# Optimization experiments

Measured on AMD Instinct MI355X. Metric: run time of the kernel, lower is better.

The kernel has to match this reference:

```python
import jax, jax.numpy as jnp
import numpy as np

B, S, E, H = 2, 2048, 1024, 16
DK = E // H
THRESHOLD = 0.1


def setup_inputs() -> dict:
    key = jax.random.key(0)
    ks = jax.random.split(key, 11)
    s = 1.0 / np.sqrt(E)
    return {
        "queries": jax.random.normal(ks[0], (B, S, E), jnp.float32),
        "keys": jax.random.normal(ks[1], (B, S, E), jnp.float32),
        "values": jax.random.normal(ks[2], (B, S, E), jnp.float32),
        "Wq": jax.random.normal(ks[3], (E, E), jnp.float32) * s,
        "bq": jnp.zeros((E,), jnp.float32),
        "Wk": jax.random.normal(ks[4], (E, E), jnp.float32) * s,
        "bk": jnp.zeros((E,), jnp.float32),
        "Wv": jax.random.normal(ks[5], (E, E), jnp.float32) * s,
        "bv": jnp.zeros((E,), jnp.float32),
        "Wp": jax.random.normal(ks[6], (E, E), jnp.float32) * s,
        "bp": jnp.zeros((E,), jnp.float32),
    }


def _split(x):
    # [B,S,E] -> [B,H,S,dk]
    return x.reshape(B, S, H, DK).transpose(0, 2, 1, 3)


def reference(queries, keys, values, Wq, bq, Wk, bk, Wv, bv, Wp, bp):
    q = _split(queries @ Wq.T + bq)
    k = _split(keys @ Wk.T + bk)
    v = _split(values @ Wv.T + bv)
    logits = jnp.einsum("bhsd,bhtd->bhst", q, k) / np.sqrt(DK)
    probs = jax.nn.softmax(logits, axis=-1)                    # [B,H,S,S]
    mask = (probs > THRESHOLD).astype(probs.dtype)
    # straight-through: value = mask*probs, grads flow via (mask*probs + probs)
    thr = mask * probs - jax.lax.stop_gradient(probs) + probs
    hidden = jnp.einsum("bhst,bhtd->bhsd", thr, v)             # [B,H,S,dk]
    merged = hidden.transpose(0, 2, 1, 3).reshape(B, S, E)
    out = merged @ Wp.T + bp
    adjacency = probs.mean(axis=1)                             # avg_attn_heads=True
    return (out, adjacency)
```

## Files before the change

### kernel.cpp

```cpp
#include <hip/hip_runtime.h>
#include <cstddef>
#include <cstdint>

constexpr size_t OUT_ELEMS = (size_t)2 * 2048 * 1024;

typedef _Float16 f16_t;
typedef __attribute__((ext_vector_type(8))) _Float16 f16x8;
typedef __attribute__((ext_vector_type(4))) float f32x4;

#define SCL2      0.1803368801111204f
#define LOG2_0P1  -3.3219280948873623f

#define EXP2F(x)  __builtin_amdgcn_exp2f(x)
#define LOG2F(x)  __builtin_amdgcn_logf(x)

#define WAITV(N)  asm volatile("s_waitcnt vmcnt(" #N ")" ::: "memory")
__device__ __forceinline__ void ringbar() {
    __builtin_amdgcn_s_barrier();
    __builtin_amdgcn_sched_barrier(0);
}

__device__ __forceinline__ f32x4 mfma16(f16x8 a, f16x8 b, f32x4 c) {
    return __builtin_amdgcn_mfma_f32_16x16x32_f16(a, b, c, 0, 0, 0);
}

__device__ __forceinline__ void gload16(const void* g, void* l) {
    __builtin_amdgcn_global_load_lds(
        (const __attribute__((address_space(1))) void*)g,
        (__attribute__((address_space(3))) void*)l, 16, 0, 0);
}

__global__ __launch_bounds__(256)
void prep_kernel(const float4* __restrict__ q, const float4* __restrict__ k,
                 const float4* __restrict__ v, const float4* __restrict__ wq,
                 const float4* __restrict__ wk, const float4* __restrict__ wv,
                 const float4* __restrict__ wp,
                 unsigned short* __restrict__ xq, unsigned short* __restrict__ xk,
                 unsigned short* __restrict__ xv, unsigned short* __restrict__ wqh,
                 unsigned short* __restrict__ wkh, unsigned short* __restrict__ wvh,
                 unsigned short* __restrict__ wph)
{
    const int z = blockIdx.y;
    const int i = blockIdx.x * 256 + threadIdx.x;
    const float4* src; unsigned short* dst; int total4;
    switch (z) {
        case 0:  src = q;  dst = xq;  total4 = 1048576; break;
        case 1:  src = k;  dst = xk;  total4 = 1048576; break;
        case 2:  src = v;  dst = xv;  total4 = 1048576; break;
        case 3:  src = wq; dst = wqh; total4 = 262144;  break;
        case 4:  src = wk; dst = wkh; total4 = 262144;  break;
        case 5:  src = wv; dst = wvh; total4 = 262144;  break;
        default: src = wp; dst = wph; total4 = 262144;  break;
    }
    if (i >= total4) return;
    const float4 v4 = src[i];
    const float vv[4] = {v4.x, v4.y, v4.z, v4.w};
    unsigned short u[4];
#pragma unroll
    for (int j = 0; j < 4; ++j) {
        f16_t h = (f16_t)vv[j];
        u[j] = __builtin_bit_cast(unsigned short, h);
    }
    uint2 w;
    w.x = u[0] | ((unsigned)u[1] << 16); w.y = u[2] | ((unsigned)u[3] << 16);
    *(uint2*)(dst + (size_t)i * 4) = w;
}

template<int OUTMODE>
__global__ __launch_bounds__(512)
void gemm_mfma(const f16_t* __restrict__ A, const f16_t* __restrict__ B,
               const float* __restrict__ bias, float scaleB,
               float* __restrict__ outF, f16_t* __restrict__ outB,
               const unsigned* __restrict__ dmask)
{
    __shared__ __align__(16) char Asl[3][16384];
    __shared__ __align__(16) char Bsl[3][16384];

    const int tid = threadIdx.x;
    const int lane = tid & 63;
    const int w = tid >> 6;
    const int wm = w >> 1;
    const int wn = w & 1;
    const int n0 = blockIdx.x * 128;
    const int m0 = blockIdx.y * 128;

    if (OUTMODE == 2) {
        const int bb = m0 >> 11;
        const int st0 = (m0 & 2047) >> 6;
        unsigned dd = 0;
        for (int hh = 0; hh < 16; ++hh)
            dd |= dmask[(bb * 16 + hh) * 32 + st0] | dmask[(bb * 16 + hh) * 32 + st0 + 1];
        if (dd == 0u) {
            const int row = tid >> 2;
            const int c0 = (tid & 3) * 32;
            float* dst = outF + (size_t)(m0 + row) * 1024 + n0 + c0;
#pragma unroll
            for (int j = 0; j < 8; ++j)
                *(float4*)(dst + j * 4) = *(const float4*)(bias + n0 + c0 + j * 4);
            return;
        }
    }

    f32x4 acc[2][4] = {};

    auto stage = [&](int ki, int buf) {
        const int kt = ki * 64;
#pragma unroll
        for (int inst = 0; inst < 2; ++inst) {
            int L = inst * 8192 + tid * 16;
            int row = L >> 7;
            int k16 = ((L >> 4) & 7) ^ (row & 7);
            gload16(A + (size_t)(m0 + row) * 1024 + kt + k16 * 8,
                    Asl[buf] + inst * 8192 + w * 1024);
            gload16(B + (size_t)(n0 + row) * 1024 + kt + k16 * 8,
                    Bsl[buf] + inst * 8192 + w * 1024);
        }
    };

    stage(0, 0);

    for (int ki = 0; ki < 16; ++ki) {
        if (ki + 1 < 16) stage(ki + 1, (ki + 1) % 3);
        if (ki < 15) { WAITV(4); } else { WAITV(0); }
        ringbar();
        const char* Ab = Asl[ki % 3];
        const char* Bb = Bsl[ki % 3];
#pragma unroll
        for (int kf = 0; kf < 2; ++kf) {
            const int k16 = kf * 4 + (lane >> 4);
            f16x8 af[2], bfr[4];
#pragma unroll
            for (int mi = 0; mi < 2; ++mi) {
                int row = wm * 32 + mi * 16 + (lane & 15);
                af[mi] = *(const f16x8*)(Ab + (row << 7) + ((k16 ^ (row & 7)) << 4));
            }
#pragma unroll
            for (int ni = 0; ni < 4; ++ni) {
                int row = wn * 64 + ni * 16 + (lane & 15);
                bfr[ni] = *(const f16x8*)(Bb + (row << 7) + ((k16 ^ (row & 7)) << 4));
            }
#pragma unroll
            for (int mi = 0; mi < 2; ++mi)
#pragma unroll
                for (int ni = 0; ni < 4; ++ni)
                    acc[mi][ni] = mfma16(af[mi], bfr[ni], acc[mi][ni]);
        }
    }

    const int crow0 = wm * 32 + (lane >> 4) * 4;
    const int ccol0 = wn * 64 + (lane & 15);
#pragma unroll
    for (int mi = 0; mi < 2; ++mi) {
#pragma unroll
        for (int ni = 0; ni < 4; ++ni) {
            const int n = n0 + ccol0 + ni * 16;
            const float bb = bias[n];
            if (OUTMODE == 2) {
#pragma unroll
                for (int r = 0; r < 4; ++r) {
                    const int m = m0 + crow0 + mi * 16 + r;
                    outF[(size_t)m * 1024 + n] = acc[mi][ni][r] + bb;
                }
            } else if (OUTMODE == 0) {
                const int h = n >> 6, d = n & 63;
#pragma unroll
                for (int r = 0; r < 4; ++r) {
                    const int m = m0 + crow0 + mi * 16 + r;
                    const int b = m >> 11, s = m & 2047;
                    const float v = acc[mi][ni][r] + bb;
                    const size_t idx = ((size_t)(b * 16 + h) * 2048 + s) * 64 + d;
                    outB[idx] = (f16_t)(v * scaleB);
                    outF[idx] = v;
                }
            } else {
                const int h = n >> 6, d = n & 63;
                const int m = m0 + crow0 + mi * 16;
                const int b = m >> 11, s = m & 2047;
                unsigned short us[4];
#pragma unroll
                for (int r = 0; r < 4; ++r) {
                    f16_t t = (f16_t)(acc[mi][ni][r] + bb);
                    us[r] = __builtin_bit_cast(unsigned short, t);
                }
                uint2 pk;
                pk.x = us[0] | ((unsigned)us[1] << 16);
                pk.y = us[2] | ((unsigned)us[3] << 16);
                *(uint2*)(outB + ((size_t)(b * 16 + h) * 64 + d) * 2048 + s) = pk;
            }
        }
    }
}

__global__ __launch_bounds__(512)
void attn_zsweep_kernel(const f16_t* __restrict__ qh, const f16_t* __restrict__ kh,
                        float2* __restrict__ partials)
{
    __shared__ __align__(16) char Klds[16384];

    const int tid = threadIdx.x;
    const int lane = tid & 63;
    const int g = lane >> 4;
    const int w = tid >> 6;
    const int tc = blockIdx.x;
    const int bh = blockIdx.y;

    {
        const size_t kbase = ((size_t)bh * 2048 + tc * 128) * 64;
#pragma unroll
        for (int inst = 0; inst < 2; ++inst) {
            int L = inst * 8192 + tid * 16;
            int row = L >> 7;
            int k16 = ((L >> 4) & 7) ^ (row & 7);
            gload16(kh + kbase + (size_t)row * 64 + k16 * 8,
                    Klds + inst * 8192 + w * 1024);
        }
    }
    __syncthreads();

    auto qload = [&](int si, f16x8& a, f16x8& b) {
        const size_t rb = ((size_t)bh * 2048 + si * 128 + w * 16 + (lane & 15)) * 64;
        a = *(const f16x8*)(qh + rb + g * 8);
        b = *(const f16x8*)(qh + rb + 32 + g * 8);
    };

    auto compute = [&](int si, f16x8 q0, f16x8 q1) {
        f32x4 acc[8] = {};
#pragma unroll
        for (int kf = 0; kf < 2; ++kf) {
            const f16x8 qf = kf ? q1 : q0;
            const int k16 = kf * 4 + g;
#pragma unroll
            for (int tg = 0; tg < 8; ++tg) {
                const int t = tg * 16 + (lane & 15);
                f16x8 bfr = *(const f16x8*)(Klds + (t << 7) + ((k16 ^ (t & 7)) << 4));
                acc[tg] = mfma16(qf, bfr, acc[tg]);
            }
        }
#pragma unroll
        for (int r = 0; r < 4; ++r) {
            float sm = 0.0f, mx = -1e30f;
#pragma unroll
            for (int tg = 0; tg < 8; ++tg) {
                const float l2 = acc[tg][r];
                sm += EXP2F(l2);
                mx = fmaxf(mx, l2);
            }
#pragma unroll
            for (int mk = 1; mk < 16; mk <<= 1) {
                sm += __shfl_xor(sm, mk);
                mx = fmaxf(mx, __shfl_xor(mx, mk));
            }
            if ((lane & 15) == 0) {
                const int srow = si * 128 + w * 16 + g * 4 + r;
                partials[((size_t)bh * 2048 + srow) * 16 + tc] = make_float2(sm, mx);
            }
        }
    };

    f16x8 qA0, qA1, qB0, qB1;
    qload(0, qA0, qA1);
    for (int si = 0; si < 16; si += 2) {
        qload(si + 1, qB0, qB1);
        compute(si, qA0, qA1);
        if (si + 2 < 16) qload(si + 2, qA0, qA1);
        compute(si + 1, qB0, qB1);
    }
}

__global__ __launch_bounds__(256)
void zred_kernel(const float2* __restrict__ partials, float* __restrict__ stats,
                 unsigned* __restrict__ dirtymask)
{
    const int tid = threadIdx.x;
    const int bh = blockIdx.y;
    const int s = blockIdx.x * 256 + tid;
    const float4* p = (const float4*)(partials + ((size_t)bh * 2048 + s) * 16);
    float sm = 0.0f, mx = -1e30f;
#pragma unroll
    for (int i = 0; i < 8; ++i) {
        const float4 v = p[i];
        sm += v.x + v.z;
        mx = fmaxf(mx, fmaxf(v.y, v.w));
    }
    const float lgZ = LOG2F(sm);
    stats[(size_t)bh * 2048 + s] = lgZ;
    const bool dirty = mx > lgZ + LOG2_0P1 - 0.10f;
    const unsigned long long m = __ballot(dirty);
    if ((tid & 63) == 0)
        dirtymask[bh * 32 + (s >> 6)] = (m != 0ull) ? 1u : 0u;
}

__global__ __launch_bounds__(256)
void attn_pv_kernel(const f16_t* __restrict__ qh, const f16_t* __restrict__ kh,
                    const f16_t* __restrict__ vT,
                    const float* __restrict__ qf32, const float* __restrict__ kf32,
                    const float* __restrict__ stats, const unsigned* __restrict__ dirtymask,
                    const float2* __restrict__ partials,
                    f16_t* __restrict__ merged)
{
    __shared__ __align__(16) char Klds[8192];
    __shared__ __align__(16) char Vlds[8192];
    __shared__ __align__(16) char Pl[4][2048];
    __shared__ unsigned cflags;

    const int tid = threadIdx.x;
    const int lane = tid & 63;
    const int g = lane >> 4;
    const int w = tid >> 6;
    const int s0 = blockIdx.x * 64;
    const int bh = blockIdx.y;
    const int b = bh >> 4, h = bh & 15;

    if (dirtymask[bh * 32 + blockIdx.x] == 0u) {
        const int row = s0 + (tid >> 2);
        f16_t* dst = merged + ((size_t)b * 2048 + row) * 1024 + h * 64 + (tid & 3) * 16;
        const uint4 z = {0u, 0u, 0u, 0u};
        *(uint4*)dst = z;
        *(uint4*)(dst + 8) = z;
        return;
    }

    f16x8 qf[2];
    float lgZ[4], lthr[4];
    {
        const size_t rowbase = ((size_t)bh * 2048 + s0 + w * 16 + (lane & 15)) * 64;
        qf[0] = *(const f16x8*)(qh + rowbase + g * 8);
        qf[1] = *(const f16x8*)(qh + rowbase + 32 + g * 8);
#pragma unroll
        for (int r = 0; r < 4; ++r) {
            lgZ[r] = stats[(size_t)bh * 2048 + s0 + w * 16 + g * 4 + r];
            lthr[r] = lgZ[r] + LOG2_0P1;
        }
    }

    if (tid == 0) cflags = 0u;
    __syncthreads();
    {
        unsigned f = 0;
#pragma unroll
        for (int r = 0; r < 4; ++r) {
            const size_t rowg = (size_t)bh * 2048 + s0 + w * 16 + g * 4 + r;
            const float thr = lthr[r] - 0.10f;
#pragma unroll
            for (int tc = 0; tc < 16; ++tc)
                if (partials[rowg * 16 + tc].y > thr) f |= (1u << tc);
        }
        if (f) atomicOr(&cflags, f);
    }
    __syncthreads();
    const unsigned flags = cflags;

    const size_t kbase = (size_t)bh * 2048 * 64;
    const size_t vbase = (size_t)bh * 64 * 2048;

    f32x4 hacc[4] = {};
    for (int tcc = 0; tcc < 2048; tcc += 64) {
        if (!((flags >> (tcc >> 7)) & 1u)) continue;
#pragma unroll
        for (int inst = 0; inst < 2; ++inst) {
            int L = inst * 4096 + tid * 16;
            int t = L >> 7;
            int k16 = ((L >> 4) & 7) ^ (t & 7);
            gload16(kh + kbase + (size_t)(tcc + t) * 64 + k16 * 8,
                    Klds + inst * 4096 + w * 1024);
            int d = t;
            gload16(vT + vbase + (size_t)d * 2048 + tcc + k16 * 8,
                    Vlds + inst * 4096 + w * 1024);
        }
        __syncthreads();

        f32x4 acc[4] = {};
#pragma unroll
        for (int kf = 0; kf < 2; ++kf) {
            const int k16 = kf * 4 + g;
            f16x8 bfr[4];
#pragma unroll
            for (int tg = 0; tg < 4; ++tg) {
                int t = tg * 16 + (lane & 15);
                bfr[tg] = *(const f16x8*)(Klds + (t << 7) + ((k16 ^ (t & 7)) << 4));
            }
#pragma unroll
            for (int tg = 0; tg < 4; ++tg)
                acc[tg] = mfma16(qf[kf], bfr[tg], acc[tg]);
        }

        char* pb = Pl[w];
        bool any = false;
#pragma unroll
        for (int tg = 0; tg < 4; ++tg)
#pragma unroll
            for (int r = 0; r < 4; ++r) {
                const float l2 = acc[tg][r];
                float p = 0.0f;
                if (l2 > lthr[r] - 0.07f) {
                    if (fabsf(l2 - lthr[r]) < 0.07f) {
                        const float* qr = qf32 + ((size_t)bh * 2048 + s0 + w * 16 + g * 4 + r) * 64;
                        const float* kr = kf32 + ((size_t)bh * 2048 + tcc + tg * 16 + (lane & 15)) * 64;
                        float dt = 0.0f;
                        for (int dd = 0; dd < 64; ++dd) dt += qr[dd] * kr[dd];
                        const float pe = EXP2F(dt * SCL2 - lgZ[r]);
                        p = (pe > 0.1f) ? pe : 0.0f;
                    } else {
                        p = EXP2F(l2 - lgZ[r]);
                    }
                }
                any |= (p != 0.0f);
                const int row = g * 4 + r;
                const int t = tg * 16 + (lane & 15);
                *(f16_t*)(pb + (row << 7) + ((2 * t) ^ ((row & 7) << 4))) = (f16_t)p;
            }

        if (__ballot(any) != 0ull) {
#pragma unroll
            for (int kf = 0; kf < 2; ++kf) {
                const int t16 = kf * 4 + g;
                f16x8 pa, vb[4];
                {
                    const int row = lane & 15;
                    pa = *(const f16x8*)(pb + (row << 7) + ((t16 ^ (row & 7)) << 4));
                }
#pragma unroll
                for (int ni = 0; ni < 4; ++ni) {
                    const int d = ni * 16 + (lane & 15);
                    vb[ni] = *(const f16x8*)(Vlds + (d << 7) + ((t16 ^ (d & 7)) << 4));
                }
#pragma unroll
                for (int ni = 0; ni < 4; ++ni)
                    hacc[ni] = mfma16(pa, vb[ni], hacc[ni]);
            }
        }
        __syncthreads();
    }

#pragma unroll
    for (int ni = 0; ni < 4; ++ni)
#pragma unroll
        for (int r = 0; r < 4; ++r) {
            const int srow = s0 + w * 16 + g * 4 + r;
            const int col = h * 64 + ni * 16 + (lane & 15);
            merged[((size_t)b * 2048 + srow) * 1024 + col] = (f16_t)hacc[ni][r];
        }
}

__global__ __launch_bounds__(256, 4)
void attn_adj_kernel(const f16_t* __restrict__ qh, const f16_t* __restrict__ kh,
                     const float* __restrict__ stats, float* __restrict__ adj)
{
    __shared__ __align__(16) char Klds[2][16384];
    __shared__ __align__(16) float Sl[16 * 64];

    const int tid = threadIdx.x;
    const int lane = tid & 63;
    const int g = lane >> 4;
    const int w = tid >> 6;
    const int t0 = blockIdx.x * 128;
    const int s0 = blockIdx.y * 64;
    const int b  = blockIdx.z;

    {
        const int hh = tid >> 4;
        const int sl = (tid * 4) & 63;
        const float4 v = *(const float4*)(stats + ((size_t)(b * 16 + hh) * 2048 + s0 + sl));
        *(float4*)&Sl[tid * 4] = v;
    }

    auto stageK = [&](int h, int buf) {
        const size_t kbase = ((size_t)(b * 16 + h) * 2048 + t0) * 64;
#pragma unroll
        for (int inst = 0; inst < 4; ++inst) {
            int L = inst * 4096 + tid * 16;
            int row = L >> 7;
            int k16 = ((L >> 4) & 7) ^ (row & 7);
            gload16(kh + kbase + (size_t)row * 64 + k16 * 8,
                    Klds[buf] + inst * 4096 + w * 1024);
        }
    };

    f32x4 aacc[8] = {};

    stageK(0, 0);
    __syncthreads();

    for (int h = 0; h < 16; ++h) {
        if (h + 1 < 16) stageK(h + 1, (h + 1) & 1);

        f16x8 q0, q1;
        {
            const size_t rb = ((size_t)(b * 16 + h) * 2048 + s0 + w * 16 + (lane & 15)) * 64;
            q0 = *(const f16x8*)(qh + rb + g * 8);
            q1 = *(const f16x8*)(qh + rb + 32 + g * 8);
        }
        float cc[4];
#pragma unroll
        for (int r = 0; r < 4; ++r)
            cc[r] = Sl[h * 64 + w * 16 + g * 4 + r] + 4.0f;

        const char* Kb = Klds[h & 1];
        f32x4 acc[8] = {};
#pragma unroll
        for (int kf = 0; kf < 2; ++kf) {
            const f16x8 qf = kf ? q1 : q0;
            const int k16 = kf * 4 + g;
#pragma unroll
            for (int tg = 0; tg < 8; ++tg) {
                const int t = tg * 16 + (lane & 15);
                const f16x8 bfr = *(const f16x8*)(Kb + (t << 7) + ((k16 ^ (t & 7)) << 4));
                acc[tg] = mfma16(qf, bfr, acc[tg]);
            }
        }
#pragma unroll
        for (int tg = 0; tg < 8; ++tg)
#pragma unroll
            for (int r = 0; r < 4; ++r)
                aacc[tg][r] += EXP2F(acc[tg][r] - cc[r]);

        __syncthreads();
    }

#pragma unroll
    for (int tg = 0; tg < 8; ++tg)
#pragma unroll
        for (int r = 0; r < 4; ++r) {
            const int s = s0 + w * 16 + g * 4 + r;
            adj[((size_t)b * 2048 + s) * 2048 + t0 + tg * 16 + (lane & 15)] = aacc[tg][r];
        }
}

extern "C" void kernel_launch(void* const* d_in, const int* in_sizes, int n_in,
                              void* d_out, int out_size, void* d_ws, size_t ws_size,
                              hipStream_t stream)
{
    (void)in_sizes; (void)n_in; (void)out_size; (void)ws_size;

    const float* queries = (const float*)d_in[0];
    const float* keys    = (const float*)d_in[1];
    const float* values  = (const float*)d_in[2];
    const float* Wq = (const float*)d_in[3];
    const float* bq = (const float*)d_in[4];
    const float* Wk = (const float*)d_in[5];
    const float* bk = (const float*)d_in[6];
    const float* Wv = (const float*)d_in[7];
    const float* bv = (const float*)d_in[8];
    const float* Wp = (const float*)d_in[9];
    const float* bp = (const float*)d_in[10];

    float* out = (float*)d_out;
    float* adj = out + OUT_ELEMS;

    char* ws = (char*)d_ws;
    f16_t* Xq   = (f16_t*)(ws);
    f16_t* Xk   = (f16_t*)(ws + 8388608);
    f16_t* Xv   = (f16_t*)(ws + 16777216);
    f16_t* Wqh  = (f16_t*)(ws + 25165824);
    f16_t* Wkh  = (f16_t*)(ws + 27262976);
    f16_t* Wvh  = (f16_t*)(ws + 29360128);
    f16_t* Wph  = (f16_t*)(ws + 31457280);
    f16_t* qh16 = (f16_t*)(ws + 33554432);
    f16_t* kh16 = (f16_t*)(ws + 41943040);
    f16_t* vT   = (f16_t*)(ws + 50331648);
    f16_t* mg   = (f16_t*)(ws + 58720256);
    float* qf32 = (float*)(ws + 67108864);
    float* kf32 = (float*)(ws + 83886080);
    float* stats = (float*)(ws + 100663296);
    float2* partials  = (float2*)(ws);
    unsigned* dirtymask = (unsigned*)(ws + 16777216 + 4194304);

    prep_kernel<<<dim3(4096, 7), 256, 0, stream>>>(
        (const float4*)queries, (const float4*)keys, (const float4*)values,
        (const float4*)Wq, (const float4*)Wk, (const float4*)Wv, (const float4*)Wp,
        (unsigned short*)Xq, (unsigned short*)Xk, (unsigned short*)Xv,
        (unsigned short*)Wqh, (unsigned short*)Wkh, (unsigned short*)Wvh,
        (unsigned short*)Wph);

    const dim3 gg(8, 32);
    gemm_mfma<0><<<gg, 512, 0, stream>>>(Xq, Wqh, bq, SCL2, qf32, qh16, nullptr);
    gemm_mfma<0><<<gg, 512, 0, stream>>>(Xk, Wkh, bk, 1.0f, kf32, kh16, nullptr);
    gemm_mfma<1><<<gg, 512, 0, stream>>>(Xv, Wvh, bv, 1.0f, nullptr, vT, nullptr);

    attn_zsweep_kernel<<<dim3(16, 32), 512, 0, stream>>>(qh16, kh16, partials);
    zred_kernel<<<dim3(8, 32), 256, 0, stream>>>(partials, stats, dirtymask);
    attn_pv_kernel<<<dim3(32, 32), 256, 0, stream>>>(qh16, kh16, vT, qf32, kf32,
                                                     stats, dirtymask, partials, mg);
    attn_adj_kernel<<<dim3(16, 32, 2), 256, 0, stream>>>(qh16, kh16, stats, adj);

    gemm_mfma<2><<<gg, 512, 0, stream>>>(mg, Wph, bp, 1.0f, out, nullptr, dirtymask);
}
```

Before: 168.2 us.

## Hold K tiles in registers for score sweeps and refine skip granularity

The row-sum sweep kernel and the adjacency kernel now keep K fragments in registers instead of staging them through LDS, which removes the shared-memory staging and the barriers. The sweep uses swapped MFMA operands so the reductions need fewer shuffles. The sweep also splits keys into 64-wide slices instead of 128-wide, so partials grow to 32 per row. The PV kernel can then skip 64-key chunks individually. The cost is more partial-statistic traffic and more redundant global Q/K loads per block in the adjacency kernel, which leans on L2.

```diff
diff --git a/kernel.cpp b/kernel.cpp
--- a/kernel.cpp
+++ b/kernel.cpp
@@ -191,70 +191,59 @@
     }
 }
 
-__global__ __launch_bounds__(512)
+__global__ __launch_bounds__(512, 4)
 void attn_zsweep_kernel(const f16_t* __restrict__ qh, const f16_t* __restrict__ kh,
                         float2* __restrict__ partials)
 {
-    __shared__ __align__(16) char Klds[16384];
-
     const int tid = threadIdx.x;
     const int lane = tid & 63;
     const int g = lane >> 4;
     const int w = tid >> 6;
-    const int tc = blockIdx.x;
-    const int bh = blockIdx.y;
-
-    {
-        const size_t kbase = ((size_t)bh * 2048 + tc * 128) * 64;
-#pragma unroll
-        for (int inst = 0; inst < 2; ++inst) {
-            int L = inst * 8192 + tid * 16;
-            int row = L >> 7;
-            int k16 = ((L >> 4) & 7) ^ (row & 7);
-            gload16(kh + kbase + (size_t)row * 64 + k16 * 8,
-                    Klds + inst * 8192 + w * 1024);
-        }
-    }
-    __syncthreads();
+    const int ts = w & 3;
+    const int sh = w >> 2;
+    const int t0 = blockIdx.x * 256 + ts * 64;
+    const int s0 = blockIdx.y * 512 + sh * 256;
+    const int bh = blockIdx.z;
+    const int slice = blockIdx.x * 4 + ts;
+
+    f16x8 kreg[2][4];
+#pragma unroll
+    for (int kf = 0; kf < 2; ++kf)
+#pragma unroll
+        for (int tg = 0; tg < 4; ++tg)
+            kreg[kf][tg] = *(const f16x8*)(kh +
+                ((size_t)bh * 2048 + t0 + tg * 16 + (lane & 15)) * 64 + kf * 32 + g * 8);
 
     auto qload = [&](int si, f16x8& a, f16x8& b) {
-        const size_t rb = ((size_t)bh * 2048 + si * 128 + w * 16 + (lane & 15)) * 64;
+        const size_t rb = ((size_t)bh * 2048 + s0 + si * 16 + (lane & 15)) * 64;
         a = *(const f16x8*)(qh + rb + g * 8);
         b = *(const f16x8*)(qh + rb + 32 + g * 8);
     };
 
     auto compute = [&](int si, f16x8 q0, f16x8 q1) {
-        f32x4 acc[8] = {};
-#pragma unroll
-        for (int kf = 0; kf < 2; ++kf) {
-            const f16x8 qf = kf ? q1 : q0;
-            const int k16 = kf * 4 + g;
-#pragma unroll
-            for (int tg = 0; tg < 8; ++tg) {
-                const int t = tg * 16 + (lane & 15);
-                f16x8 bfr = *(const f16x8*)(Klds + (t << 7) + ((k16 ^ (t & 7)) << 4));
-                acc[tg] = mfma16(qf, bfr, acc[tg]);
-            }
-        }
-#pragma unroll
-        for (int r = 0; r < 4; ++r) {
-            float sm = 0.0f, mx = -1e30f;
-#pragma unroll
-            for (int tg = 0; tg < 8; ++tg) {
-                const float l2 = acc[tg][r];
-                sm += EXP2F(l2);
-                mx = fmaxf(mx, l2);
-            }
-#pragma unroll
-            for (int mk = 1; mk < 16; mk <<= 1) {
-                sm += __shfl_xor(sm, mk);
-                mx = fmaxf(mx, __shfl_xor(mx, mk));
-            }
-            if ((lane & 15) == 0) {
-                const int srow = si * 128 + w * 16 + g * 4 + r;
-                partials[((size_t)bh * 2048 + srow) * 16 + tc] = make_float2(sm, mx);
-            }
-        }
+        f32x4 acc[4] = {};
+#pragma unroll
+        for (int tg = 0; tg < 4; ++tg) {
+            acc[tg] = mfma16(kreg[0][tg], q0, acc[tg]);
+            acc[tg] = mfma16(kreg[1][tg], q1, acc[tg]);
+        }
+        float sms[4] = {0.0f, 0.0f, 0.0f, 0.0f};
+        float mxs[4] = {-1e30f, -1e30f, -1e30f, -1e30f};
+#pragma unroll
+        for (int tg = 0; tg < 4; ++tg)
+#pragma unroll
+            for (int r = 0; r < 4; ++r) {
+                sms[r] += EXP2F(acc[tg][r]);
+                mxs[r] = fmaxf(mxs[r], acc[tg][r]);
+            }
+        float sm = (sms[0] + sms[1]) + (sms[2] + sms[3]);
+        float mx = fmaxf(fmaxf(mxs[0], mxs[1]), fmaxf(mxs[2], mxs[3]));
+        sm += __shfl_xor(sm, 16); sm += __shfl_xor(sm, 32);
+        mx = fmaxf(mx, __shfl_xor(mx, 16));
+        mx = fmaxf(mx, __shfl_xor(mx, 32));
+        if (g == 0)
+            partials[((size_t)bh * 2048 + s0 + si * 16 + (lane & 15)) * 32 + slice]
+                = make_float2(sm, mx);
     };
 
     f16x8 qA0, qA1, qB0, qB1;
@@ -274,10 +263,10 @@
     const int tid = threadIdx.x;
     const int bh = blockIdx.y;
     const int s = blockIdx.x * 256 + tid;
-    const float4* p = (const float4*)(partials + ((size_t)bh * 2048 + s) * 16);
+    const float4* p = (const float4*)(partials + ((size_t)bh * 2048 + s) * 32);
     float sm = 0.0f, mx = -1e30f;
 #pragma unroll
-    for (int i = 0; i < 8; ++i) {
+    for (int i = 0; i < 16; ++i) {
         const float4 v = p[i];
         sm += v.x + v.z;
         mx = fmaxf(mx, fmaxf(v.y, v.w));
@@ -342,8 +331,8 @@
             const size_t rowg = (size_t)bh * 2048 + s0 + w * 16 + g * 4 + r;
             const float thr = lthr[r] - 0.10f;
 #pragma unroll
-            for (int tc = 0; tc < 16; ++tc)
-                if (partials[rowg * 16 + tc].y > thr) f |= (1u << tc);
+            for (int tc = 0; tc < 32; ++tc)
+                if (partials[rowg * 32 + tc].y > thr) f |= (1u << tc);
         }
         if (f) atomicOr(&cflags, f);
     }
@@ -355,7 +344,7 @@
 
     f32x4 hacc[4] = {};
     for (int tcc = 0; tcc < 2048; tcc += 64) {
-        if (!((flags >> (tcc >> 7)) & 1u)) continue;
+        if (!((flags >> (tcc >> 6)) & 1u)) continue;
 #pragma unroll
         for (int inst = 0; inst < 2; ++inst) {
             int L = inst * 4096 + tid * 16;
@@ -446,84 +435,55 @@
 void attn_adj_kernel(const f16_t* __restrict__ qh, const f16_t* __restrict__ kh,
                      const float* __restrict__ stats, float* __restrict__ adj)
 {
-    __shared__ __align__(16) char Klds[2][16384];
-    __shared__ __align__(16) float Sl[16 * 64];
-
     const int tid = threadIdx.x;
     const int lane = tid & 63;
     const int g = lane >> 4;
     const int w = tid >> 6;
-    const int t0 = blockIdx.x * 128;
+    const int t0 = blockIdx.x * 128 + w * 32;
     const int s0 = blockIdx.y * 64;
     const int b  = blockIdx.z;
 
-    {
-        const int hh = tid >> 4;
-        const int sl = (tid * 4) & 63;
-        const float4 v = *(const float4*)(stats + ((size_t)(b * 16 + hh) * 2048 + s0 + sl));
-        *(float4*)&Sl[tid * 4] = v;
-    }
-
-    auto stageK = [&](int h, int buf) {
-        const size_t kbase = ((size_t)(b * 16 + h) * 2048 + t0) * 64;
-#pragma unroll
-        for (int inst = 0; inst < 4; ++inst) {
-            int L = inst * 4096 + tid * 16;
-            int row = L >> 7;
-            int k16 = ((L >> 4) & 7) ^ (row & 7);
-            gload16(kh + kbase + (size_t)row * 64 + k16 * 8,
-                    Klds[buf] + inst * 4096 + w * 1024);
-        }
-    };
-
-    f32x4 aacc[8] = {};
-
-    stageK(0, 0);
-    __syncthreads();
+    f32x4 aacc[4][2] = {};
 
     for (int h = 0; h < 16; ++h) {
-        if (h + 1 < 16) stageK(h + 1, (h + 1) & 1);
-
-        f16x8 q0, q1;
-        {
-            const size_t rb = ((size_t)(b * 16 + h) * 2048 + s0 + w * 16 + (lane & 15)) * 64;
-            q0 = *(const f16x8*)(qh + rb + g * 8);
-            q1 = *(const f16x8*)(qh + rb + 32 + g * 8);
-        }
-        float cc[4];
-#pragma unroll
-        for (int r = 0; r < 4; ++r)
-            cc[r] = Sl[h * 64 + w * 16 + g * 4 + r] + 4.0f;
-
-        const char* Kb = Klds[h & 1];
-        f32x4 acc[8] = {};
-#pragma unroll
-        for (int kf = 0; kf < 2; ++kf) {
-            const f16x8 qf = kf ? q1 : q0;
-            const int k16 = kf * 4 + g;
-#pragma unroll
-            for (int tg = 0; tg < 8; ++tg) {
-                const int t = tg * 16 + (lane & 15);
-                const f16x8 bfr = *(const f16x8*)(Kb + (t << 7) + ((k16 ^ (t & 7)) << 4));
-                acc[tg] = mfma16(qf, bfr, acc[tg]);
-            }
-        }
-#pragma unroll
-        for (int tg = 0; tg < 8; ++tg)
-#pragma unroll
-            for (int r = 0; r < 4; ++r)
-                aacc[tg][r] += EXP2F(acc[tg][r] - cc[r]);
-
-        __syncthreads();
-    }
-
-#pragma unroll
-    for (int tg = 0; tg < 8; ++tg)
-#pragma unroll
-        for (int r = 0; r < 4; ++r) {
-            const int s = s0 + w * 16 + g * 4 + r;
-            adj[((size_t)b * 2048 + s) * 2048 + t0 + tg * 16 + (lane & 15)] = aacc[tg][r];
-        }
+        const int bh = b * 16 + h;
+        f16x8 kreg[2][2];
+#pragma unroll
+        for (int kf = 0; kf < 2; ++kf)
+#pragma unroll
+            for (int tg = 0; tg < 2; ++tg)
+                kreg[kf][tg] = *(const f16x8*)(kh +
+                    ((size_t)bh * 2048 + t0 + tg * 16 + (lane & 15)) * 64 + kf * 32 + g * 8);
+
+#pragma unroll
+        for (int sg = 0; sg < 4; ++sg) {
+            const size_t qb = ((size_t)bh * 2048 + s0 + sg * 16 + (lane & 15)) * 64;
+            const f16x8 q0 = *(const f16x8*)(qh + qb + g * 8);
+            const f16x8 q1 = *(const f16x8*)(qh + qb + 32 + g * 8);
+            f32x4 acc[2] = {};
+#pragma unroll
+            for (int tg = 0; tg < 2; ++tg) {
+                acc[tg] = mfma16(q0, kreg[0][tg], acc[tg]);
+                acc[tg] = mfma16(q1, kreg[1][tg], acc[tg]);
+            }
+            const f32x4 cc = *(const f32x4*)(stats + (size_t)bh * 2048 + s0 + sg * 16 + g * 4);
+#pragma unroll
+            for (int tg = 0; tg < 2; ++tg)
+#pragma unroll
+                for (int r = 0; r < 4; ++r)
+                    aacc[sg][tg][r] += EXP2F(acc[tg][r] - cc[r] - 4.0f);
+        }
+    }
+
+#pragma unroll
+    for (int sg = 0; sg < 4; ++sg)
+#pragma unroll
+        for (int tg = 0; tg < 2; ++tg)
+#pragma unroll
+            for (int r = 0; r < 4; ++r) {
+                const int s = s0 + sg * 16 + g * 4 + r;
+                adj[((size_t)b * 2048 + s) * 2048 + t0 + tg * 16 + (lane & 15)] = aacc[sg][tg][r];
+            }
 }
 
 extern "C" void kernel_launch(void* const* d_in, const int* in_sizes, int n_in,
@@ -563,7 +523,7 @@
     float* kf32 = (float*)(ws + 83886080);
     float* stats = (float*)(ws + 100663296);
     float2* partials  = (float2*)(ws);
-    unsigned* dirtymask = (unsigned*)(ws + 16777216 + 4194304);
+    unsigned* dirtymask = (unsigned*)(ws + 16777216);
 
     prep_kernel<<<dim3(4096, 7), 256, 0, stream>>>(
         (const float4*)queries, (const float4*)keys, (const float4*)values,
@@ -577,7 +537,7 @@
     gemm_mfma<0><<<gg, 512, 0, stream>>>(Xk, Wkh, bk, 1.0f, kf32, kh16, nullptr);
     gemm_mfma<1><<<gg, 512, 0, stream>>>(Xv, Wvh, bv, 1.0f, nullptr, vT, nullptr);
 
-    attn_zsweep_kernel<<<dim3(16, 32), 512, 0, stream>>>(qh16, kh16, partials);
+    attn_zsweep_kernel<<<dim3(8, 4, 32), 512, 0, stream>>>(qh16, kh16, partials);
     zred_kernel<<<dim3(8, 32), 256, 0, stream>>>(partials, stats, dirtymask);
     attn_pv_kernel<<<dim3(32, 32), 256, 0, stream>>>(qh16, kh16, vT, qf32, kf32,
                                                      stats, dirtymask, partials, mg);
```

Measured after the change: 233.6 us. +38.8%, slower.
